# Kernel optimization log

Hardware: AMD Instinct MI355X
Metric: run time of the kernel (lower is better)

Reference implementation:

```python
import jax, jax.numpy as jnp
import numpy as np

N_NODES = 100000
N_EDGES = 1600000
IN_DIM = 128
HID = 128
OUT_DIM = 2
NUM_GRAPHS = 64
BN_EPS = 1e-5


def _glorot(key, shape):
    fan_in, fan_out = shape[0], shape[1]
    lim = np.sqrt(6.0 / (fan_in + fan_out))
    return jax.random.uniform(key, shape, jnp.float32, -lim, lim)


def setup_inputs() -> dict:
    key = jax.random.key(0)
    ks = jax.random.split(key, 12)
    x = jax.random.normal(ks[0], (N_NODES, IN_DIM), jnp.float32)
    edge_index = jax.random.randint(ks[1], (2, N_EDGES), 0, N_NODES, jnp.int64)
    batch = jnp.sort(jax.random.randint(ks[2], (N_NODES,), 0, NUM_GRAPHS, jnp.int64))
    return {
        "x": x,
        "edge_index": edge_index,
        "batch": batch,
        "W1": _glorot(ks[3], (IN_DIM, HID)), "b1": jnp.zeros((HID,), jnp.float32),
        "g1": jnp.ones((HID,), jnp.float32), "be1": jnp.zeros((HID,), jnp.float32),
        "W2": _glorot(ks[4], (HID, HID)), "b2": jnp.zeros((HID,), jnp.float32),
        "g2": jnp.ones((HID,), jnp.float32), "be2": jnp.zeros((HID,), jnp.float32),
        "Wc1": _glorot(ks[5], (HID, HID // 2)), "bc1": jnp.zeros((HID // 2,), jnp.float32),
        "Wc2": _glorot(ks[6], (HID // 2, OUT_DIM)), "bc2": jnp.zeros((OUT_DIM,), jnp.float32),
    }


def gcn_conv(x, src, dst, W, b):
    # PyG GCNConv: add self-loops, symmetric deg^{-1/2} normalization
    n = x.shape[0]
    loop = jnp.arange(n, dtype=src.dtype)
    s = jnp.concatenate([src, loop])
    d = jnp.concatenate([dst, loop])
    deg = jax.ops.segment_sum(jnp.ones_like(d, dtype=x.dtype), d, num_segments=n)
    dinv = jnp.where(deg > 0, jax.lax.rsqrt(deg), 0.0)
    xw = x @ W  # [N, out]
    msgs = xw[s] * (dinv[s] * dinv[d])[:, None]  # [E+N, out]
    out = jax.ops.segment_sum(msgs, d, num_segments=n)
    return out + b


def batchnorm(x, gamma, beta):
    mean = jnp.mean(x, axis=0)
    var = jnp.mean(jnp.square(x - mean), axis=0)  # biased, as torch BN
    return (x - mean) * jax.lax.rsqrt(var + BN_EPS) * gamma + beta


def reference(x, edge_index, batch, W1, b1, g1, be1, W2, b2, g2, be2, Wc1, bc1, Wc2, bc2):
    src, dst = edge_index[0], edge_index[1]
    x = jnp.nan_to_num(x, nan=0.0)
    # layer 1: GCNConv -> BN -> ReLU (dropout = identity in eval)
    h = jax.nn.relu(batchnorm(gcn_conv(x, src, dst, W1, b1), g1, be1))
    # layer 2
    h = jax.nn.relu(batchnorm(gcn_conv(h, src, dst, W2, b2), g2, be2))
    # global mean pool per graph
    sums = jax.ops.segment_sum(h, batch, num_segments=NUM_GRAPHS)
    counts = jax.ops.segment_sum(jnp.ones((h.shape[0],), h.dtype), batch, num_segments=NUM_GRAPHS)
    pooled = sums / jnp.maximum(counts, 1.0)[:, None]  # [G, HID]
    # classifier MLP
    z = jax.nn.relu(pooled @ Wc1 + bc1)
    out = z @ Wc2 + bc2
    return jnp.nan_to_num(out, nan=0.0)
```

## Files before the change

### kernel.cpp

```cpp
#include <hip/hip_runtime.h>

typedef unsigned int uint;
typedef unsigned short ushort;

#define HID 128
#define NGRAPH 64

typedef __attribute__((ext_vector_type(8))) short short8;
typedef __attribute__((ext_vector_type(4))) float floatx4;

__device__ __forceinline__ float bflo(uint w){ return __uint_as_float(w<<16); }
__device__ __forceinline__ float bfhi(uint w){ return __uint_as_float(w & 0xffff0000u); }
__device__ __forceinline__ float bf2f(ushort u){ return __uint_as_float(((uint)u)<<16); }
__device__ __forceinline__ ushort f2bf(float f){
  uint u = __float_as_uint(f);
  u = u + 0x7fffu + ((u>>16)&1u);
  return (ushort)(u>>16);
}
__device__ __forceinline__ uint pack2(float a, float b){
  return (uint)f2bf(a) | ((uint)f2bf(b)<<16);
}
__device__ __forceinline__ float nanz(float v){ return (v==v) ? v : 0.f; }

__device__ __forceinline__ int bat(const int* b, int i, int is64){
  return is64 ? b[2*(size_t)i] : b[i];
}

__global__ void k_prep(int* __restrict__ cnt, float* __restrict__ stats1,
                       float* __restrict__ stats2, float* __restrict__ pooled,
                       uint* __restrict__ xwzero, int NN,
                       const int* __restrict__ ei, int* __restrict__ flags,
                       const float* __restrict__ W1, const float* __restrict__ W2,
                       ushort* __restrict__ wt1, ushort* __restrict__ wt2,
                       int* __restrict__ src32, int* __restrict__ dst32, int E){
  int bid = blockIdx.x;
  if (bid < 512){
    int i = bid*256 + threadIdx.x;
    for (int t = i; t < NN; t += 512*256) cnt[t] = 0;
    if (i < 256){ stats1[i] = 0.f; stats2[i] = 0.f; }
    if (i < NGRAPH*HID) pooled[i] = 0.f;
    if (i < 64) xwzero[i] = 0u;
    if (bid == 0 && threadIdx.x < 64){
      int t = threadIdx.x;
      bool nz = (ei[2*t + 1] != 0) || (ei[2*(t+64) + 1] != 0);
      unsigned long long m = __ballot(nz);
      if (t == 0) flags[1] = (m == 0ULL) ? 1 : 0;
    }
  } else if (bid < 520){
    int b = bid - 512;
    const float* W  = (b & 1) ? W2  : W1;
    ushort*      Wt = (b & 1) ? wt2 : wt1;
    int base = (b >> 1)*4096;
    for (int o = base + threadIdx.x; o < base + 4096; o += 256){
      int j    = o & 7;
      int lane = (o >> 3) & 63;
      int ct   = (o >> 9) & 7;
      int ks   = o >> 12;
      int k = ks*32 + (lane >> 4)*8 + j;
      int n = ct*16 + (lane & 15);
      Wt[o] = f2bf(W[(size_t)k*HID + n]);
    }
  } else {
    __shared__ int is64s;
    if (threadIdx.x < 64){
      bool nz = (ei[2*threadIdx.x + 1] != 0);
      unsigned long long m = __ballot(nz);
      if (threadIdx.x == 0) is64s = (m == 0ULL) ? 1 : 0;
    }
    __syncthreads();
    int is64 = is64s;
    int b = bid - 520;
    if (is64){
      for (int e = b*256 + (int)threadIdx.x; e < E; e += 512*256){
        src32[e] = ei[2*(size_t)e];
        dst32[e] = ei[2*((size_t)E + e)];
      }
    } else {
      for (int e = b*256 + (int)threadIdx.x; e < E; e += 512*256){
        src32[e] = ei[e];
        dst32[e] = ei[(size_t)E + e];
      }
    }
  }
}

__global__ void k_sentinel(ushort* out, int n){
  int i = blockIdx.x*blockDim.x + threadIdx.x;
  if (i < n) out[i] = 0x429A;
}


#define NCHUNK 256

__global__ __launch_bounds__(256) void k_hist(const int* __restrict__ dst32,
    int* __restrict__ cnt, int E, int NN){
  int part  = blockIdx.x & 7;
  int chunk = blockIdx.x >> 3;
  int p0 = (int)(((long long)NN *  part   ) >> 3);
  int p1 = (int)(((long long)NN * (part+1)) >> 3);
  int per = (E + NCHUNK - 1) / NCHUNK;
  int e0 = chunk * per;
  int e1 = e0 + per; if (e1 > E) e1 = E;
  for (int e = e0 + (int)threadIdx.x; e < e1; e += 256){
    int d = dst32[e];
    if (d >= p0 && d < p1) atomicAdd(&cnt[d], 1);
  }
}

__global__ __launch_bounds__(256) void k_scatter(const int* __restrict__ src32,
    const int* __restrict__ dst32, int* __restrict__ cursor,
    int* __restrict__ srclist, int E, int NN){
  int part  = blockIdx.x & 7;
  int chunk = blockIdx.x >> 3;
  int p0 = (int)(((long long)NN *  part   ) >> 3);
  int p1 = (int)(((long long)NN * (part+1)) >> 3);
  int per = (E + NCHUNK - 1) / NCHUNK;
  int e0 = chunk * per;
  int e1 = e0 + per; if (e1 > E) e1 = E;
  for (int e = e0 + (int)threadIdx.x; e < e1; e += 256){
    int d = dst32[e];
    if (d >= p0 && d < p1){
      int s = src32[e];
      if ((uint)s < (uint)NN)
        srclist[atomicAdd(&cursor[d], 1)] = s;
    }
  }
}

__global__ void k_scan1(const int* __restrict__ cnt, int* __restrict__ partials,
                        float* __restrict__ dinv, int NN){
  int t = threadIdx.x;
  int base = blockIdx.x*1024 + t*4;
  int v0=0,v1=0,v2=0,v3=0;
  if (base + 3 < NN){ int4 v = *(const int4*)(cnt + base); v0=v.x; v1=v.y; v2=v.z; v3=v.w; }
  else {
    if (base+0 < NN) v0 = cnt[base+0];
    if (base+1 < NN) v1 = cnt[base+1];
    if (base+2 < NN) v2 = cnt[base+2];
    if (base+3 < NN) v3 = cnt[base+3];
  }
  if (base+0 < NN) dinv[base+0] = rsqrtf((float)(v0+1));
  if (base+1 < NN) dinv[base+1] = rsqrtf((float)(v1+1));
  if (base+2 < NN) dinv[base+2] = rsqrtf((float)(v2+1));
  if (base+3 < NN) dinv[base+3] = rsqrtf((float)(v3+1));
  __shared__ int red[256];
  red[t] = v0+v1+v2+v3;
  __syncthreads();
  for (int off=128; off>0; off>>=1){
    if (t < off) red[t] += red[t+off];
    __syncthreads();
  }
  if (t==0) partials[blockIdx.x] = red[0];
}

__global__ void k_scan3(const int* __restrict__ cnt, const int* __restrict__ partials,
                        int* __restrict__ offs, int* __restrict__ cursor, int NN){
  int t = threadIdx.x;
  __shared__ int red2[256];
  int lp = 0;
  for (int i = t; i < (int)blockIdx.x; i += 256) lp += partials[i];
  red2[t] = lp;
  __syncthreads();
  for (int off=128; off>0; off>>=1){
    if (t < off) red2[t] += red2[t+off];
    __syncthreads();
  }
  int pbase = red2[0];
  if (t == 0 && blockIdx.x == gridDim.x-1)
    offs[NN] = pbase + partials[blockIdx.x];
  __syncthreads();

  int base = blockIdx.x*1024 + t*4;
  int v0=0,v1=0,v2=0,v3=0;
  if (base + 3 < NN){ int4 v = *(const int4*)(cnt + base); v0=v.x; v1=v.y; v2=v.z; v3=v.w; }
  else {
    if (base+0 < NN) v0 = cnt[base+0];
    if (base+1 < NN) v1 = cnt[base+1];
    if (base+2 < NN) v2 = cnt[base+2];
    if (base+3 < NN) v3 = cnt[base+3];
  }
  int tsum = v0+v1+v2+v3;
  __shared__ int sc[256];
  sc[t] = tsum;
  __syncthreads();
  for (int off=1; off<256; off<<=1){
    int val = (t >= off) ? sc[t-off] : 0;
    __syncthreads();
    sc[t] += val;
    __syncthreads();
  }
  int run = pbase + sc[t] - tsum;
  if (base+0 < NN){ offs[base+0] = run; cursor[base+0] = run; run += v0; }
  if (base+1 < NN){ offs[base+1] = run; cursor[base+1] = run; run += v1; }
  if (base+2 < NN){ offs[base+2] = run; cursor[base+2] = run; run += v2; }
  if (base+3 < NN){ offs[base+3] = run; cursor[base+3] = run; run += v3; }
}


__global__ __launch_bounds__(256) void k_gemm1(const float* __restrict__ A,
    const ushort* __restrict__ Wt, const float* __restrict__ dinv,
    ushort* __restrict__ O, int NN){
  __shared__ ushort wlds[16384];
  int tid = threadIdx.x;
  {
    const uint4* s = (const uint4*)Wt;
    uint4* d = (uint4*)wlds;
    #pragma unroll
    for (int i = 0; i < 8; i++) d[tid + i*256] = s[tid + i*256];
  }
  __syncthreads();
  int wave = tid >> 6, lane = tid & 63, m = lane & 15, q = lane >> 4;
  int rowbase = blockIdx.x*64 + wave*16;
  int ar = rowbase + m; if (ar >= NN) ar = NN-1;
  const float* arow = A + (size_t)ar*HID;
  short8 af[4];
  #pragma unroll
  for (int ks=0; ks<4; ks++){
    int kb = ks*32 + q*8;
    float4 f0 = *(const float4*)(arow + kb);
    float4 f1 = *(const float4*)(arow + kb + 4);
    short8 t;
    t[0]=(short)f2bf(nanz(f0.x)); t[1]=(short)f2bf(nanz(f0.y));
    t[2]=(short)f2bf(nanz(f0.z)); t[3]=(short)f2bf(nanz(f0.w));
    t[4]=(short)f2bf(nanz(f1.x)); t[5]=(short)f2bf(nanz(f1.y));
    t[6]=(short)f2bf(nanz(f1.z)); t[7]=(short)f2bf(nanz(f1.w));
    af[ks] = t;
  }
  floatx4 acc[8];
  #pragma unroll
  for (int ct=0; ct<8; ct++) acc[ct] = (floatx4){0.f,0.f,0.f,0.f};
  #pragma unroll
  for (int ks=0; ks<4; ks++){
    #pragma unroll
    for (int ct=0; ct<8; ct++){
      short8 bfrag = *(const short8*)&wlds[(((ks*8+ct)*64) + lane)*8];
      acc[ct] = __builtin_amdgcn_mfma_f32_16x16x32_bf16(af[ks], bfrag, acc[ct], 0, 0, 0);
    }
  }
  float dv[4];
  #pragma unroll
  for (int i=0;i<4;i++){ int r = rowbase + q*4 + i; dv[i] = (r < NN) ? dinv[r] : 0.f; }
  #pragma unroll
  for (int ct=0; ct<8; ct++){
    #pragma unroll
    for (int i=0;i<4;i++){
      int r = rowbase + q*4 + i;
      if (r < NN) O[(size_t)r*HID + ct*16 + m] = f2bf(acc[ct][i]*dv[i]);
    }
  }
}


__global__ __launch_bounds__(256) void k_gemm2(const uint* __restrict__ agg,
    const float* __restrict__ stats, const float* __restrict__ gam,
    const float* __restrict__ bet, const ushort* __restrict__ Wt,
    const float* __restrict__ dinv, ushort* __restrict__ O, int NN, float invn){
  __shared__ ushort wlds[16384];
  __shared__ float cA[128], cB[128];
  int tid = threadIdx.x;
  {
    const uint4* s = (const uint4*)Wt;
    uint4* d = (uint4*)wlds;
    #pragma unroll
    for (int i = 0; i < 8; i++) d[tid + i*256] = s[tid + i*256];
    if (tid < 128){
      float sm = stats[tid], sq = stats[128+tid];
      float mean = sm*invn;
      float var = fmaxf(sq*invn - mean*mean, 0.f);
      float a = gam[tid] * rsqrtf(var + 1e-5f);
      cA[tid] = a;
      cB[tid] = bet[tid] - mean*a;
    }
  }
  __syncthreads();
  int wave = tid >> 6, lane = tid & 63, m = lane & 15, q = lane >> 4;
  int rowbase = blockIdx.x*64 + wave*16;
  int ar = rowbase + m; if (ar >= NN) ar = NN-1;
  const uint* arow = agg + (size_t)ar*64;
  short8 af[4];
  #pragma unroll
  for (int ks=0; ks<4; ks++){
    int kb = ks*32 + q*8;
    uint4 u = *(const uint4*)(arow + (kb >> 1));
    short8 t;
    uint uw[4] = {u.x, u.y, u.z, u.w};
    #pragma unroll
    for (int p=0; p<4; p++){
      int k0 = kb + 2*p;
      float v0 = fmaxf(cA[k0]  *bflo(uw[p]) + cB[k0],   0.f);
      float v1 = fmaxf(cA[k0+1]*bfhi(uw[p]) + cB[k0+1], 0.f);
      t[2*p]   = (short)f2bf(v0);
      t[2*p+1] = (short)f2bf(v1);
    }
    af[ks] = t;
  }
  floatx4 acc[8];
  #pragma unroll
  for (int ct=0; ct<8; ct++) acc[ct] = (floatx4){0.f,0.f,0.f,0.f};
  #pragma unroll
  for (int ks=0; ks<4; ks++){
    #pragma unroll
    for (int ct=0; ct<8; ct++){
      short8 bfrag = *(const short8*)&wlds[(((ks*8+ct)*64) + lane)*8];
      acc[ct] = __builtin_amdgcn_mfma_f32_16x16x32_bf16(af[ks], bfrag, acc[ct], 0, 0, 0);
    }
  }
  float dv[4];
  #pragma unroll
  for (int i=0;i<4;i++){ int r = rowbase + q*4 + i; dv[i] = (r < NN) ? dinv[r] : 0.f; }
  #pragma unroll
  for (int ct=0; ct<8; ct++){
    #pragma unroll
    for (int i=0;i<4;i++){
      int r = rowbase + q*4 + i;
      if (r < NN) O[(size_t)r*HID + ct*16 + m] = f2bf(acc[ct][i]*dv[i]);
    }
  }
}


__global__ __launch_bounds__(256) void k_agg(const uint* __restrict__ xw,
    const int* __restrict__ offs, const int* __restrict__ srclist,
    const float* __restrict__ dinv, uint* __restrict__ agg,
    float* __restrict__ stats, int NN){
  __shared__ float lstat[256];
  lstat[threadIdx.x] = 0.f;
  __syncthreads();
  int wib = threadIdx.x >> 6;
  int lane = threadIdx.x & 63;
  int wid = blockIdx.x*4 + wib;
  int nw = gridDim.x*4;
  float s0=0.f, s1=0.f, q0=0.f, q1=0.f;
  for (int n = wid; n < NN; n += nw){
    int lo = offs[n], hi = offs[n+1];
    float dvn = dinv[n];
    float a0 = 0.f, a1 = 0.f;
    for (int base = lo; base < hi; base += 64){
      int c = hi - base; if (c > 64) c = 64;
      int sidx = (lane < c) ? srclist[base + lane] : NN;
      for (int jb = 0; jb < c; jb += 8){
        uint w[8];
        #pragma unroll
        for (int t = 0; t < 8; t++){
          int sj = __shfl(sidx, jb + t, 64);
          w[t] = xw[(size_t)sj*64 + lane];
        }
        #pragma unroll
        for (int t = 0; t < 8; t++){
          a0 += bflo(w[t]);
          a1 += bfhi(w[t]);
        }
      }
    }
    uint wsf = xw[(size_t)n*64 + lane];
    a0 = (a0 + bflo(wsf)) * dvn;
    a1 = (a1 + bfhi(wsf)) * dvn;
    agg[(size_t)n*64 + lane] = pack2(a0, a1);
    s0 += a0; s1 += a1; q0 += a0*a0; q1 += a1*a1;
  }
  int ch = lane*2;
  atomicAdd(&lstat[ch],       s0);
  atomicAdd(&lstat[ch+1],     s1);
  atomicAdd(&lstat[128+ch],   q0);
  atomicAdd(&lstat[128+ch+1], q1);
  __syncthreads();
  atomicAdd(&stats[threadIdx.x], lstat[threadIdx.x]);
}


#define PSPLIT 16

__global__ __launch_bounds__(256) void k_pool(const uint* __restrict__ agg32,
    const int* __restrict__ batch, const float* __restrict__ stats,
    const float* __restrict__ gam, const float* __restrict__ bet,
    float* __restrict__ pooled, int* __restrict__ counts,
    int NN, const int* __restrict__ flags, float invn){
  int is64 = flags[1];
  __shared__ int bounds[2];
  __shared__ float cA[128], cB[128];
  int g  = blockIdx.x;
  int si = blockIdx.y;
  int tid = threadIdx.x;
  if (tid < 128){
    float sm = stats[tid], sq = stats[128+tid];
    float mean = sm*invn;
    float var = fmaxf(sq*invn - mean*mean, 0.f);
    float a = gam[tid] * rsqrtf(var + 1e-5f);
    cA[tid] = a;
    cB[tid] = bet[tid] - mean*a;
  }
  if (tid == 0){
    int lo=0, hi=NN;
    while (lo<hi){ int mid=(lo+hi)>>1; if (bat(batch,mid,is64) < g) lo=mid+1; else hi=mid; }
    bounds[0] = lo;
    int lo2=lo, hi2=NN;
    while (lo2<hi2){ int mid=(lo2+hi2)>>1; if (bat(batch,mid,is64) < g+1) lo2=mid+1; else hi2=mid; }
    bounds[1] = lo2;
    if (si == 0) counts[g] = hi2 - lo;
  }
  __syncthreads();
  int lo = bounds[0], hi = bounds[1];
  int cnt = hi - lo;
  int chunk = (cnt + PSPLIT - 1) / PSPLIT;
  int s = lo + si*chunk;
  int e = s + chunk; if (e > hi) e = hi;
  int lane = tid & 63, rg = tid >> 6;
  int ch = lane*2;
  float a0c = cA[ch],   b0c = cB[ch];
  float a1c = cA[ch+1], b1c = cB[ch+1];
  float acc0 = 0.f, acc1 = 0.f;
  for (int r = s + rg; r < e; r += 4){
    uint w = agg32[(size_t)r*64 + lane];
    acc0 += fmaxf(a0c*bflo(w) + b0c, 0.f);
    acc1 += fmaxf(a1c*bfhi(w) + b1c, 0.f);
  }
  __shared__ float red[512];
  red[tid] = acc0;
  red[256+tid] = acc1;
  __syncthreads();
  if (tid < 64){
    float s0 = red[tid] + red[tid+64] + red[tid+128] + red[tid+192];
    float s1 = red[256+tid] + red[320+tid] + red[384+tid] + red[448+tid];
    atomicAdd(&pooled[g*HID + ch],     s0);
    atomicAdd(&pooled[g*HID + ch + 1], s1);
  }
}


__global__ void k_mlp(const float* __restrict__ pooled, const int* __restrict__ counts,
                      const float* __restrict__ Wc1, const float* __restrict__ bc1,
                      const float* __restrict__ Wc2, const float* __restrict__ bc2,
                      float* __restrict__ out){
  __shared__ float P[NGRAPH*HID];
  __shared__ float Z[NGRAPH*64];
  int tid = threadIdx.x;
  for (int i = tid; i < NGRAPH*HID; i += 256){
    int g = i >> 7;
    float c = (float)counts[g];
    P[i] = pooled[i] / fmaxf(c, 1.f);
  }
  __syncthreads();
  for (int idx = tid; idx < NGRAPH*64; idx += 256){
    int g = idx >> 6, j = idx & 63;
    float acc = bc1[j];
    for (int k = 0; k < HID; k++) acc += P[g*HID + k] * Wc1[k*64 + j];
    Z[idx] = fmaxf(acc, 0.f);
  }
  __syncthreads();
  if (tid < NGRAPH*2){
    int g = tid >> 1, o = tid & 1;
    float acc = bc2[o];
    for (int k = 0; k < 64; k++) acc += Z[g*64 + k] * Wc2[k*2 + o];
    out[tid] = nanz(acc);
  }
}

extern "C" void kernel_launch(void* const* d_in, const int* in_sizes, int n_in,
                              void* d_out, int out_size, void* d_ws, size_t ws_size,
                              hipStream_t stream){
  const float* x   = (const float*)d_in[0];
  const int*   ei  = (const int*)d_in[1];
  const int* batch = (const int*)d_in[2];
  const float* W1  = (const float*)d_in[3];
  const float* g1  = (const float*)d_in[5];
  const float* be1 = (const float*)d_in[6];
  const float* W2  = (const float*)d_in[7];
  const float* g2  = (const float*)d_in[9];
  const float* be2 = (const float*)d_in[10];
  const float* Wc1 = (const float*)d_in[11];
  const float* bc1 = (const float*)d_in[12];
  const float* Wc2 = (const float*)d_in[13];
  const float* bc2 = (const float*)d_in[14];

  const int NN = in_sizes[2];
  const int E  = in_sizes[1] / 2;

  char* p = (char*)d_ws;
  auto carve = [&](size_t bytes)->char*{
    char* r = p; p += (bytes + 255) & ~(size_t)255; return r;
  };
  int NPART = (NN + 1023)/1024;
  int*   flags    = (int*)  carve(64*4);
  int*   cnt      = (int*)  carve((size_t)NN*4);
  int*   cursor   = (int*)  carve(((size_t)NN+1)*4);
  int*   offs     = (int*)  carve(((size_t)NN+1)*4);
  int*   partials = (int*)  carve((size_t)NPART*4);
  int*   srclist  = (int*)  carve((size_t)E*4);
  int*   src32    = (int*)  carve((size_t)E*4);
  int*   dst32    = (int*)  carve((size_t)E*4);
  float* dinv     = (float*)carve((size_t)NN*4);
  float* stats1   = (float*)carve(256*4);
  float* stats2   = (float*)carve(256*4);
  float* pooled   = (float*)carve((size_t)NGRAPH*HID*4);
  int*   counts   = (int*)  carve(NGRAPH*4);
  ushort* wt1     = (ushort*)carve(16384*2);
  ushort* wt2     = (ushort*)carve(16384*2);
  ushort* xw      = (ushort*)carve(((size_t)NN+1)*HID*2);
  ushort* agg     = (ushort*)carve((size_t)NN*HID*2);
  if ((size_t)(p - (char*)d_ws) > ws_size){
    k_sentinel<<<(out_size+255)/256, 256, 0, stream>>>((ushort*)d_out, out_size);
    return;
  }

  const float invn = 1.f/(float)NN;

  k_prep   <<<1032, 256, 0, stream>>>(cnt, stats1, stats2, pooled,
                                      (uint*)(xw + (size_t)NN*HID), NN, ei, flags,
                                      W1, W2, wt1, wt2, src32, dst32, E);

  k_hist   <<<NCHUNK*8, 256, 0, stream>>>(dst32, cnt, E, NN);
  k_scan1  <<<NPART, 256, 0, stream>>>(cnt, partials, dinv, NN);
  k_scan3  <<<NPART, 256, 0, stream>>>(cnt, partials, offs, cursor, NN);
  k_scatter<<<NCHUNK*8, 256, 0, stream>>>(src32, dst32, cursor, srclist, E, NN);

  int gblocks = (NN + 63)/64;
  k_gemm1<<<gblocks, 256, 0, stream>>>(x, wt1, dinv, xw, NN);
  k_agg  <<<2048, 256, 0, stream>>>((const uint*)xw, offs, srclist, dinv, (uint*)agg, stats1, NN);
  k_gemm2<<<gblocks, 256, 0, stream>>>((const uint*)agg, stats1, g1, be1, wt2, dinv, xw, NN, invn);
  k_agg  <<<2048, 256, 0, stream>>>((const uint*)xw, offs, srclist, dinv, (uint*)agg, stats2, NN);
  k_pool <<<dim3(NGRAPH, PSPLIT), 256, 0, stream>>>((const uint*)agg, batch, stats2, g2, be2,
                                                    pooled, counts, NN, flags, invn);
  k_mlp  <<<1, 256, 0, stream>>>(pooled, counts, Wc1, bc1, Wc2, bc2, (float*)d_out);
}
```

Before: 550.2 us.

## Pre-bucket edges by destination partition before histogram and scatter

Replaces the int64-to-int32 edge conversion and the 8-way filtered rescans of all edges in the histogram and scatter kernels with a bucketing kernel. It writes (src,dst) pairs into 8 destination-range buckets, so histogram and scatter each read only their own partition instead of scanning the full edge list eight times. It adds a bucket pass with local and global atomics and a fixed per-bucket capacity, which could silently drop edges if one partition overflows.

```diff
diff --git a/kernel.cpp b/kernel.cpp
--- a/kernel.cpp
+++ b/kernel.cpp
@@ -30,9 +30,9 @@
                        float* __restrict__ stats2, float* __restrict__ pooled,
                        uint* __restrict__ xwzero, int NN,
                        const int* __restrict__ ei, int* __restrict__ flags,
+                       int* __restrict__ bcnt,
                        const float* __restrict__ W1, const float* __restrict__ W2,
-                       ushort* __restrict__ wt1, ushort* __restrict__ wt2,
-                       int* __restrict__ src32, int* __restrict__ dst32, int E){
+                       ushort* __restrict__ wt1, ushort* __restrict__ wt2){
   int bid = blockIdx.x;
   if (bid < 512){
     int i = bid*256 + threadIdx.x;
@@ -40,13 +40,14 @@
     if (i < 256){ stats1[i] = 0.f; stats2[i] = 0.f; }
     if (i < NGRAPH*HID) pooled[i] = 0.f;
     if (i < 64) xwzero[i] = 0u;
+    if (i < 8)  bcnt[i] = 0;
     if (bid == 0 && threadIdx.x < 64){
       int t = threadIdx.x;
       bool nz = (ei[2*t + 1] != 0) || (ei[2*(t+64) + 1] != 0);
       unsigned long long m = __ballot(nz);
       if (t == 0) flags[1] = (m == 0ULL) ? 1 : 0;
     }
-  } else if (bid < 520){
+  } else {
     int b = bid - 512;
     const float* W  = (b & 1) ? W2  : W1;
     ushort*      Wt = (b & 1) ? wt2 : wt1;
@@ -60,27 +61,6 @@
       int n = ct*16 + (lane & 15);
       Wt[o] = f2bf(W[(size_t)k*HID + n]);
     }
-  } else {
-    __shared__ int is64s;
-    if (threadIdx.x < 64){
-      bool nz = (ei[2*threadIdx.x + 1] != 0);
-      unsigned long long m = __ballot(nz);
-      if (threadIdx.x == 0) is64s = (m == 0ULL) ? 1 : 0;
-    }
-    __syncthreads();
-    int is64 = is64s;
-    int b = bid - 520;
-    if (is64){
-      for (int e = b*256 + (int)threadIdx.x; e < E; e += 512*256){
-        src32[e] = ei[2*(size_t)e];
-        dst32[e] = ei[2*((size_t)E + e)];
-      }
-    } else {
-      for (int e = b*256 + (int)threadIdx.x; e < E; e += 512*256){
-        src32[e] = ei[e];
-        dst32[e] = ei[(size_t)E + e];
-      }
-    }
   }
 }
 
@@ -90,40 +70,69 @@
 }
 
 
-#define NCHUNK 256
-
-__global__ __launch_bounds__(256) void k_hist(const int* __restrict__ dst32,
-    int* __restrict__ cnt, int E, int NN){
+#define BBLK 512
+
+__global__ __launch_bounds__(256) void k_bucket(const int* __restrict__ ei,
+    const int* __restrict__ flags, int2* __restrict__ pairs,
+    int* __restrict__ bcnt, int E, int NN, int CAP){
+  int is64 = flags[1];
+  int per = (E + BBLK - 1)/BBLK;
+  int e0 = blockIdx.x*per;
+  int e1 = e0 + per; if (e1 > E) e1 = E;
+  __shared__ int lcnt[8], lbase[8], lpos[8];
+  if (threadIdx.x < 8){ lcnt[threadIdx.x] = 0; lpos[threadIdx.x] = 0; }
+  __syncthreads();
+  const int* dstp = ei + (is64 ? 2*(size_t)E : (size_t)E);
+  for (int e = e0 + (int)threadIdx.x; e < e1; e += 256){
+    int d = is64 ? dstp[2*(size_t)e] : dstp[e];
+    int s = is64 ? ei[2*(size_t)e]   : ei[e];
+    if ((uint)d < (uint)NN && (uint)s < (uint)NN){
+      int part = (int)(((long long)d*8)/NN);
+      atomicAdd(&lcnt[part], 1);
+    }
+  }
+  __syncthreads();
+  if (threadIdx.x < 8)
+    lbase[threadIdx.x] = atomicAdd(&bcnt[threadIdx.x], lcnt[threadIdx.x]);
+  __syncthreads();
+  for (int e = e0 + (int)threadIdx.x; e < e1; e += 256){
+    int d = is64 ? dstp[2*(size_t)e] : dstp[e];
+    int s = is64 ? ei[2*(size_t)e]   : ei[e];
+    if ((uint)d < (uint)NN && (uint)s < (uint)NN){
+      int part = (int)(((long long)d*8)/NN);
+      int slot = lbase[part] + atomicAdd(&lpos[part], 1);
+      if (slot < CAP) pairs[(size_t)part*CAP + slot] = make_int2(s, d);
+    }
+  }
+}
+
+
+#define HCH 64
+
+__global__ __launch_bounds__(256) void k_hist(const int2* __restrict__ pairs,
+    const int* __restrict__ bcnt, int* __restrict__ cnt, int CAP){
   int part  = blockIdx.x & 7;
   int chunk = blockIdx.x >> 3;
-  int p0 = (int)(((long long)NN *  part   ) >> 3);
-  int p1 = (int)(((long long)NN * (part+1)) >> 3);
-  int per = (E + NCHUNK - 1) / NCHUNK;
-  int e0 = chunk * per;
-  int e1 = e0 + per; if (e1 > E) e1 = E;
-  for (int e = e0 + (int)threadIdx.x; e < e1; e += 256){
-    int d = dst32[e];
-    if (d >= p0 && d < p1) atomicAdd(&cnt[d], 1);
-  }
-}
-
-__global__ __launch_bounds__(256) void k_scatter(const int* __restrict__ src32,
-    const int* __restrict__ dst32, int* __restrict__ cursor,
-    int* __restrict__ srclist, int E, int NN){
+  int n = bcnt[part]; if (n > CAP) n = CAP;
+  int per = (n + HCH - 1)/HCH;
+  int i0 = chunk*per, i1 = i0 + per; if (i1 > n) i1 = n;
+  const int2* pp = pairs + (size_t)part*CAP;
+  for (int i = i0 + (int)threadIdx.x; i < i1; i += 256)
+    atomicAdd(&cnt[pp[i].y], 1);
+}
+
+__global__ __launch_bounds__(256) void k_scatter(const int2* __restrict__ pairs,
+    const int* __restrict__ bcnt, int* __restrict__ cursor,
+    int* __restrict__ srclist, int CAP){
   int part  = blockIdx.x & 7;
   int chunk = blockIdx.x >> 3;
-  int p0 = (int)(((long long)NN *  part   ) >> 3);
-  int p1 = (int)(((long long)NN * (part+1)) >> 3);
-  int per = (E + NCHUNK - 1) / NCHUNK;
-  int e0 = chunk * per;
-  int e1 = e0 + per; if (e1 > E) e1 = E;
-  for (int e = e0 + (int)threadIdx.x; e < e1; e += 256){
-    int d = dst32[e];
-    if (d >= p0 && d < p1){
-      int s = src32[e];
-      if ((uint)s < (uint)NN)
-        srclist[atomicAdd(&cursor[d], 1)] = s;
-    }
+  int n = bcnt[part]; if (n > CAP) n = CAP;
+  int per = (n + HCH - 1)/HCH;
+  int i0 = chunk*per, i1 = i0 + per; if (i1 > n) i1 = n;
+  const int2* pp = pairs + (size_t)part*CAP;
+  for (int i = i0 + (int)threadIdx.x; i < i1; i += 256){
+    int2 pr = pp[i];
+    srclist[atomicAdd(&cursor[pr.y], 1)] = pr.x;
   }
 }
 
@@ -474,6 +483,7 @@
 
   const int NN = in_sizes[2];
   const int E  = in_sizes[1] / 2;
+  const int CAP = E/8 + 32768;
 
   char* p = (char*)d_ws;
   auto carve = [&](size_t bytes)->char*{
@@ -481,13 +491,13 @@
   };
   int NPART = (NN + 1023)/1024;
   int*   flags    = (int*)  carve(64*4);
+  int*   bcnt     = (int*)  carve(64*4);
   int*   cnt      = (int*)  carve((size_t)NN*4);
   int*   cursor   = (int*)  carve(((size_t)NN+1)*4);
   int*   offs     = (int*)  carve(((size_t)NN+1)*4);
   int*   partials = (int*)  carve((size_t)NPART*4);
   int*   srclist  = (int*)  carve((size_t)E*4);
-  int*   src32    = (int*)  carve((size_t)E*4);
-  int*   dst32    = (int*)  carve((size_t)E*4);
+  int2*  pairs    = (int2*) carve((size_t)8*CAP*8);
   float* dinv     = (float*)carve((size_t)NN*4);
   float* stats1   = (float*)carve(256*4);
   float* stats2   = (float*)carve(256*4);
@@ -504,14 +514,15 @@
 
   const float invn = 1.f/(float)NN;
 
-  k_prep   <<<1032, 256, 0, stream>>>(cnt, stats1, stats2, pooled,
-                                      (uint*)(xw + (size_t)NN*HID), NN, ei, flags,
-                                      W1, W2, wt1, wt2, src32, dst32, E);
-
-  k_hist   <<<NCHUNK*8, 256, 0, stream>>>(dst32, cnt, E, NN);
+  k_prep   <<<520, 256, 0, stream>>>(cnt, stats1, stats2, pooled,
+                                     (uint*)(xw + (size_t)NN*HID), NN, ei, flags,
+                                     bcnt, W1, W2, wt1, wt2);
+  k_bucket <<<BBLK, 256, 0, stream>>>(ei, flags, pairs, bcnt, E, NN, CAP);
+
+  k_hist   <<<8*HCH, 256, 0, stream>>>(pairs, bcnt, cnt, CAP);
   k_scan1  <<<NPART, 256, 0, stream>>>(cnt, partials, dinv, NN);
   k_scan3  <<<NPART, 256, 0, stream>>>(cnt, partials, offs, cursor, NN);
-  k_scatter<<<NCHUNK*8, 256, 0, stream>>>(src32, dst32, cursor, srclist, E, NN);
+  k_scatter<<<8*HCH, 256, 0, stream>>>(pairs, bcnt, cursor, srclist, CAP);
 
   int gblocks = (NN + 63)/64;
   k_gemm1<<<gblocks, 256, 0, stream>>>(x, wt1, dinv, xw, NN);
```

Measured after the change: 564.8 us. +2.7%, slower.
